# Kernel tuning notes

Measured on AMD Instinct MI355X. Metric: run time of the kernel, lower is better.

## Reference

```python
import jax, jax.numpy as jnp
import numpy as np
from jax import lax

B, C_IN, T = 1024, 9, 2048
RT = T // 4            # reduced timesteps after two MaxPool(2)
HID, OUT = 128, 64
N_NODES = B * RT


def _chain_edges(rt, batch):
    """Bidirectional chain graph per sample, offset per batch element (PyG fallback)."""
    i = np.arange(rt - 1)
    src = np.concatenate([i, i + 1])   # edge_index[0] = source j
    dst = np.concatenate([i + 1, i])   # edge_index[1] = target i
    off = (np.arange(batch) * rt)[:, None]
    src = (src[None, :] + off).reshape(-1)
    dst = (dst[None, :] + off).reshape(-1)
    # degree with self-loops (GCNConv adds self-loops): endpoints 2, interior 3
    deg = np.full(rt, 3.0, np.float32)
    deg[0] = deg[-1] = 2.0
    deg = np.tile(deg, batch)
    return jnp.asarray(src, jnp.int32), jnp.asarray(dst, jnp.int32), jnp.asarray(deg ** -0.5)


def _conv1d(x, w, b):
    # x: [B, Cin, T], w: [Cout, Cin, 5] -> [B, Cout, T] (padding=2)
    y = lax.conv_general_dilated(x, w, window_strides=(1,), padding=[(2, 2)],
                                 dimension_numbers=('NCH', 'OIH', 'NCH'))
    return y + b[None, :, None]


def _maxpool2(x):
    b, c, t = x.shape
    return x.reshape(b, c, t // 2, 2).max(axis=-1)


def _gcn(x, W, b, src, dst, dinv):
    # GCNConv: x' = D^-1/2 (A+I) D^-1/2 (x W) + b
    h = x @ W                                        # [N, F]
    norm_e = (dinv[src] * dinv[dst])[:, None]        # per-edge sym norm
    agg = jax.ops.segment_sum(h[src] * norm_e, dst, num_segments=h.shape[0])
    return agg + h * (dinv * dinv)[:, None] + b      # self-loop term: 1/deg


def setup_inputs() -> dict:
    key = jax.random.key(0)
    ks = jax.random.split(key, 12)
    s = lambda k, shp, sc: jax.random.normal(k, shp, jnp.float32) * sc
    return {
        'x': jax.random.normal(ks[0], (B, C_IN, T), jnp.float32),
        'conv1_w': s(ks[1], (16, C_IN, 5), 0.15), 'conv1_b': jnp.zeros((16,), jnp.float32),
        'conv2_w': s(ks[2], (32, 16, 5), 0.1),   'conv2_b': jnp.zeros((32,), jnp.float32),
        'gcn1_w': s(ks[3], (32, HID), 0.17),     'gcn1_b': jnp.zeros((HID,), jnp.float32),
        'gcn2_w': s(ks[4], (HID, HID), 0.09),    'gcn2_b': jnp.zeros((HID,), jnp.float32),
        'fc_w': s(ks[5], (HID, OUT), 0.09),      'fc_b': jnp.zeros((OUT,), jnp.float32),
    }


def reference(x, conv1_w, conv1_b, conv2_w, conv2_b,
              gcn1_w, gcn1_b, gcn2_w, gcn2_b, fc_w, fc_b):
    b, c, t = x.shape
    h = _maxpool2(jax.nn.relu(_conv1d(x, conv1_w, conv1_b)))   # [B,16,T/2]
    h = _maxpool2(jax.nn.relu(_conv1d(h, conv2_w, conv2_b)))   # [B,32,T/4]
    rt = h.shape[-1]
    h = jnp.transpose(h, (0, 2, 1)).reshape(b * rt, 32)        # [N,32]
    src, dst, dinv = _chain_edges(rt, b)
    h = jax.nn.relu(_gcn(h, gcn1_w, gcn1_b, src, dst, dinv))
    h = jax.nn.relu(_gcn(h, gcn2_w, gcn2_b, src, dst, dinv))
    h = h.reshape(b, rt, -1).mean(axis=1)                      # [B,HID]
    return h @ fc_w + fc_b                                     # [B,OUT]
```

## Files before the change

### kernel.cpp

```cpp
#include <hip/hip_runtime.h>
#include <hip/hip_bf16.h>

#define B_      1024
#define CIN     9
#define T0_     2048
#define C1_     16
#define C2_     32
#define RT_     512
#define NNODES  (B_ * RT_)
#define HID_    128
#define OUTF_   64

typedef __attribute__((ext_vector_type(8))) __bf16 bf16x8;
typedef __attribute__((ext_vector_type(4))) float f32x4;
typedef __attribute__((ext_vector_type(8))) unsigned short us8;

__device__ __forceinline__ float bf2f(unsigned short u) {
    union { unsigned int i; float f; } c; c.i = ((unsigned int)u) << 16; return c.f;
}
__device__ __forceinline__ unsigned short f2bf(float f) {
    union { float f; unsigned int i; } c; c.f = f;
    unsigned int i = c.i + 0x7FFFu + ((c.i >> 16) & 1u);
    return (unsigned short)(i >> 16);
}
__device__ __forceinline__ float dinv_of(int r) {
    return (r == 0 || r == RT_ - 1) ? 0.70710678118f : 0.57735026919f;
}

__global__ __launch_bounds__(256) void repack_w(
    const float* __restrict__ W1g, const float* __restrict__ W2g,
    const float* __restrict__ Wc1g, const float* __restrict__ Wc2g,
    unsigned short* __restrict__ Wb1, unsigned short* __restrict__ Wb2,
    unsigned short* __restrict__ Wc1, unsigned short* __restrict__ Wc2)
{
    const int tid = threadIdx.x;
    const int bid = blockIdx.x;
    if (bid == 0) {
        for (int s = tid; s < 32 * 128; s += 256) {
            int k = s >> 7, f = s & 127;
            int lane = ((k >> 3) << 4) + (f & 15);
            int e = (((f >> 4) * 64) + lane) * 8 + (k & 7);
            Wb1[e] = f2bf(W1g[s]);
        }
    } else if (bid <= 4) {
        const int s0 = (bid - 1) * 4096;
        for (int i = tid; i < 4096; i += 256) {
            int s = s0 + i;
            int k = s >> 7, f = s & 127;
            int ks = k >> 5, lane = (((k >> 3) & 3) << 4) + (f & 15);
            int e = ((ks * 8 + (f >> 4)) * 64 + lane) * 8 + (k & 7);
            Wb2[e] = f2bf(W2g[s]);
        }
    } else if (bid == 5) {
        for (int e = tid; e < 3 * 64 * 8; e += 256) {
            int j = e & 7, lane = (e >> 3) & 63, ks = e >> 9;
            int kk = ks * 32 + (lane >> 4) * 8 + j;
            int k = kk >> 4, ci = kk & 15, co = lane & 15;
            Wc1[e] = (k < 5 && ci < CIN) ? f2bf(Wc1g[(co * CIN + ci) * 5 + k]) : 0;
        }
    } else {
        for (int e = tid; e < 3 * 2 * 64 * 8; e += 256) {
            int j = e & 7, lane = (e >> 3) & 63, nt = (e >> 9) & 1, ks = e >> 10;
            int kk = ks * 32 + (lane >> 4) * 8 + j;
            int k = kk >> 4, ci = kk & 15, co = nt * 16 + (lane & 15);
            Wc2[e] = (k < 5) ? f2bf(Wc2g[(co * C1_ + ci) * 5 + k]) : 0;
        }
    }
}

__global__ __launch_bounds__(256, 2) void mega(
    const float* __restrict__ x,
    const unsigned short* __restrict__ Wc1,
    const unsigned short* __restrict__ Wc2,
    const unsigned short* __restrict__ Wb1,
    const unsigned short* __restrict__ Wb2,
    const float* __restrict__ c1b, const float* __restrict__ c2b,
    const float* __restrict__ g1b, const float* __restrict__ g2b,
    float* __restrict__ partials)
{
    __shared__ __align__(16) unsigned char lds[75808];
    unsigned short* xs    = (unsigned short*)(lds);
    unsigned short* As1   = (unsigned short*)(lds);
    unsigned short* y2loc = (unsigned short*)(lds + 11520);
    unsigned short* A2    = (unsigned short*)(lds);
    unsigned short* y1ext = (unsigned short*)(lds + 39424);
    unsigned short* H     = (unsigned short*)(lds + 39424);
    float* bls1 = (float*)(lds + 74784);
    float* bls2 = (float*)(lds + 75296);

    const int tid = threadIdx.x;
    const int b = blockIdx.x >> 2;
    const int r0 = (blockIdx.x & 3) * 128;
    const int n0 = blockIdx.x * 128;
    if (tid < 128) { bls1[tid] = g1b[tid]; bls2[tid] = g2b[tid]; }

    const int lane = tid & 63, wave = tid >> 6;
    const int m = lane & 15, q = lane >> 4;

    {
        const float* xb = x + (size_t)b * CIN * T0_;
        const int xbase = 4 * r0 - 14;
        for (int s = tid; s < 552; s += 256) {
            const int xt = xbase + s;
            us8 o0, o1;
            if (xt >= 0 && xt < T0_) {
                #pragma unroll
                for (int ci = 0; ci < 8; ci++) o0[ci] = f2bf(xb[ci * T0_ + xt]);
                o1[0] = f2bf(xb[8 * T0_ + xt]);
                #pragma unroll
                for (int jj = 1; jj < 8; jj++) o1[jj] = 0;
            } else {
                #pragma unroll
                for (int jj = 0; jj < 8; jj++) { o0[jj] = 0; o1[jj] = 0; }
            }
            *(us8*)(xs + s * 24) = o0;
            *(us8*)(xs + s * 24 + 8) = o1;
        }
    }
    __syncthreads();

    {
        bf16x8 wf[3];
        #pragma unroll
        for (int ks = 0; ks < 3; ks++) wf[ks] = *(const bf16x8*)(Wc1 + (ks * 64 + lane) * 8);
        const float bv = c1b[m];
        const int t1base = 2 * r0 - 6;
        for (int mt = wave; mt < 34; mt += 4) {
            f32x4 acc = {};
            #pragma unroll
            for (int ks = 0; ks < 3; ks++) {
                const int row = mt * 16 + m + ks * 2 + (q >> 1);
                const bf16x8 af = *(const bf16x8*)(xs + row * 24 + (q & 1) * 8);
                acc = __builtin_amdgcn_mfma_f32_16x16x32_bf16(af, wf[ks], acc, 0, 0, 0);
            }
            const int prow = mt * 8 + q * 2;
            const int t1a = t1base + prow, t1b = t1a + 1;
            const float p0 = fmaxf(fmaxf(acc[0], acc[1]) + bv, 0.f);
            const float p1 = fmaxf(fmaxf(acc[2], acc[3]) + bv, 0.f);
            if (prow < 268)
                y1ext[prow * 16 + m] = (t1a >= 0 && t1a < 1024) ? f2bf(p0) : (unsigned short)0;
            if (prow + 1 < 268)
                y1ext[(prow + 1) * 16 + m] = (t1b >= 0 && t1b < 1024) ? f2bf(p1) : (unsigned short)0;
        }
        for (int idx = tid; idx < 192; idx += 256) y1ext[268 * 16 + idx] = 0;
    }
    __syncthreads();

    {
        bf16x8 wf[3][2];
        #pragma unroll
        for (int ks = 0; ks < 3; ks++)
            #pragma unroll
            for (int nt = 0; nt < 2; nt++)
                wf[ks][nt] = *(const bf16x8*)(Wc2 + ((ks * 2 + nt) * 64 + lane) * 8);
        const float bv0 = c2b[m], bv1 = c2b[16 + m];
        for (int mt = wave; mt < 17; mt += 4) {
            f32x4 a0 = {}, a1 = {};
            #pragma unroll
            for (int ks = 0; ks < 3; ks++) {
                const int row = mt * 16 + m + ks * 2 + (q >> 1);
                const bf16x8 af = *(const bf16x8*)(y1ext + row * 16 + (q & 1) * 8);
                a0 = __builtin_amdgcn_mfma_f32_16x16x32_bf16(af, wf[ks][0], a0, 0, 0, 0);
                a1 = __builtin_amdgcn_mfma_f32_16x16x32_bf16(af, wf[ks][1], a1, 0, 0, 0);
            }
            const int nrow = mt * 8 + q * 2;
            if (nrow < 132) {
                y2loc[nrow * 32 + m]      = f2bf(fmaxf(fmaxf(a0[0], a0[1]) + bv0, 0.f));
                y2loc[nrow * 32 + 16 + m] = f2bf(fmaxf(fmaxf(a1[0], a1[1]) + bv1, 0.f));
            }
            if (nrow + 1 < 132) {
                y2loc[(nrow + 1) * 32 + m]      = f2bf(fmaxf(fmaxf(a0[2], a0[3]) + bv0, 0.f));
                y2loc[(nrow + 1) * 32 + 16 + m] = f2bf(fmaxf(fmaxf(a1[2], a1[3]) + bv1, 0.f));
            }
        }
    }
    __syncthreads();

    for (int s = tid; s < 288; s += 256) {
        const int i = s >> 1, fh = (s & 1) * 16;
        unsigned short* dst = As1 + i * 40 + fh;
        const int r = r0 - 1 + i;
        if (i >= 130 || r < 0 || r >= RT_) {
            us8 z;
            #pragma unroll
            for (int j = 0; j < 8; j++) z[j] = 0;
            *(us8*)dst = z; *(us8*)(dst + 8) = z;
        } else {
            const float dm = dinv_of(r), cm = dm * dm;
            const unsigned short* Yc = y2loc + (i + 1) * 32 + fh;
            us8 c0 = *(const us8*)(Yc), c1 = *(const us8*)(Yc + 8);
            float v[16];
            #pragma unroll
            for (int j = 0; j < 8; j++) { v[j] = cm * bf2f(c0[j]); v[8 + j] = cm * bf2f(c1[j]); }
            if (r > 0) {
                const float cl = dm * dinv_of(r - 1);
                us8 a0 = *(const us8*)(Yc - 32), a1 = *(const us8*)(Yc - 24);
                #pragma unroll
                for (int j = 0; j < 8; j++) { v[j] += cl * bf2f(a0[j]); v[8 + j] += cl * bf2f(a1[j]); }
            }
            if (r < RT_ - 1) {
                const float cr = dm * dinv_of(r + 1);
                us8 a0 = *(const us8*)(Yc + 32), a1 = *(const us8*)(Yc + 40);
                #pragma unroll
                for (int j = 0; j < 8; j++) { v[j] += cr * bf2f(a0[j]); v[8 + j] += cr * bf2f(a1[j]); }
            }
            us8 o0, o1;
            #pragma unroll
            for (int j = 0; j < 8; j++) { o0[j] = f2bf(v[j]); o1[j] = f2bf(v[8 + j]); }
            *(us8*)dst = o0; *(us8*)(dst + 8) = o1;
        }
    }
    __syncthreads();

    {
        const int ft0 = wave * 2;
        const bf16x8 wf0 = *(const bf16x8*)(Wb1 + (ft0 * 64 + lane) * 8);
        const bf16x8 wf1 = *(const bf16x8*)(Wb1 + ((ft0 + 1) * 64 + lane) * 8);
        const float4 bv0 = *(const float4*)&bls1[ft0 * 16 + q * 4];
        const float4 bv1 = *(const float4*)&bls1[(ft0 + 1) * 16 + q * 4];
        #pragma unroll
        for (int nt = 0; nt < 9; nt++) {
            const bf16x8 bfr = *(const bf16x8*)(As1 + (nt * 16 + m) * 40 + q * 8);
            f32x4 a0 = {}, a1 = {};
            a0 = __builtin_amdgcn_mfma_f32_16x16x32_bf16(wf0, bfr, a0, 0, 0, 0);
            a1 = __builtin_amdgcn_mfma_f32_16x16x32_bf16(wf1, bfr, a1, 0, 0, 0);
            const int row = nt * 16 + m;
            if (row < 130) {
                ushort4 o0, o1;
                o0.x = f2bf(fmaxf(a0[0] + bv0.x, 0.f));
                o0.y = f2bf(fmaxf(a0[1] + bv0.y, 0.f));
                o0.z = f2bf(fmaxf(a0[2] + bv0.z, 0.f));
                o0.w = f2bf(fmaxf(a0[3] + bv0.w, 0.f));
                o1.x = f2bf(fmaxf(a1[0] + bv1.x, 0.f));
                o1.y = f2bf(fmaxf(a1[1] + bv1.y, 0.f));
                o1.z = f2bf(fmaxf(a1[2] + bv1.z, 0.f));
                o1.w = f2bf(fmaxf(a1[3] + bv1.w, 0.f));
                *(ushort4*)(H + row * 136 + ft0 * 16 + q * 4) = o0;
                *(ushort4*)(H + row * 136 + (ft0 + 1) * 16 + q * 4) = o1;
            }
        }
    }
    __syncthreads();

    {
        const int j = tid >> 1, fh = (tid & 1) * 64;
        const int r = r0 + j;
        const float dm = dinv_of(r), cm = dm * dm;
        const float cl = (r > 0) ? dm * dinv_of(r - 1) : 0.f;
        const float cr = (r < RT_ - 1) ? dm * dinv_of(r + 1) : 0.f;
        const unsigned short* Hl = H + j * 136 + fh;
        const unsigned short* Hc = Hl + 136;
        const unsigned short* Hr = Hc + 136;
        unsigned short* dst = A2 + j * 152 + fh;
        #pragma unroll
        for (int c = 0; c < 8; c++) {
            us8 cc = *(const us8*)(Hc + c * 8);
            us8 ll = *(const us8*)(Hl + c * 8);
            us8 rr = *(const us8*)(Hr + c * 8);
            us8 o;
            #pragma unroll
            for (int e = 0; e < 8; e++)
                o[e] = f2bf(cm * bf2f(cc[e]) + cl * bf2f(ll[e]) + cr * bf2f(rr[e]));
            *(us8*)(dst + c * 8) = o;
        }
    }
    __syncthreads();

    bf16x8 bw[4][2];
    #pragma unroll
    for (int ks = 0; ks < 4; ks++)
        #pragma unroll
        for (int i = 0; i < 2; i++) {
            int ct = wave * 2 + i;
            bw[ks][i] = *(const bf16x8*)(Wb2 + ((size_t)((ks * 8 + ct) * 64 + lane)) * 8);
        }
    f32x4 acc[8][2] = {};
    #pragma unroll
    for (int ks = 0; ks < 4; ks++) {
        #pragma unroll
        for (int nt = 0; nt < 8; nt++) {
            const bf16x8 af = *(const bf16x8*)(A2 + (nt * 16 + m) * 152 + ks * 32 + q * 8);
            acc[nt][0] = __builtin_amdgcn_mfma_f32_16x16x32_bf16(af, bw[ks][0], acc[nt][0], 0, 0, 0);
            acc[nt][1] = __builtin_amdgcn_mfma_f32_16x16x32_bf16(af, bw[ks][1], acc[nt][1], 0, 0, 0);
        }
    }
    const float bb0 = bls2[wave * 32 + m];
    const float bb1 = bls2[wave * 32 + 16 + m];
    float s0 = 0.f, s1 = 0.f;
    #pragma unroll
    for (int nt = 0; nt < 8; nt++)
        #pragma unroll
        for (int rgi = 0; rgi < 4; rgi++) {
            s0 += fmaxf(acc[nt][0][rgi] + bb0, 0.f);
            s1 += fmaxf(acc[nt][1][rgi] + bb1, 0.f);
        }
    s0 += __shfl_xor(s0, 16, 64); s0 += __shfl_xor(s0, 32, 64);
    s1 += __shfl_xor(s1, 16, 64); s1 += __shfl_xor(s1, 32, 64);
    if (lane < 16) {
        float* p = partials + (size_t)blockIdx.x * 128 + wave * 32;
        p[m] = s0;
        p[16 + m] = s1;
    }
}

__global__ __launch_bounds__(128) void fc_kernel(
    const float* __restrict__ partials, const float* __restrict__ fw,
    const float* __restrict__ fb, float* __restrict__ out)
{
    __shared__ float sm[128];
    const int b = blockIdx.x, tid = threadIdx.x;
    float s = 0.f;
    #pragma unroll
    for (int t = 0; t < 4; t++) s += partials[((b << 2) + t) * 128 + tid];
    sm[tid] = s * (1.0f / 512.0f);
    __syncthreads();
    if (tid < 64) {
        float acc = fb[tid];
        #pragma unroll 8
        for (int f = 0; f < 128; f++) acc += sm[f] * fw[f * 64 + tid];
        out[b * 64 + tid] = acc;
    }
}

extern "C" void kernel_launch(void* const* d_in, const int* in_sizes, int n_in,
                              void* d_out, int out_size, void* d_ws, size_t ws_size,
                              hipStream_t stream)
{
    const float* x   = (const float*)d_in[0];
    const float* w1  = (const float*)d_in[1];
    const float* b1  = (const float*)d_in[2];
    const float* w2  = (const float*)d_in[3];
    const float* b2  = (const float*)d_in[4];
    const float* g1w = (const float*)d_in[5];
    const float* g1b = (const float*)d_in[6];
    const float* g2w = (const float*)d_in[7];
    const float* g2b = (const float*)d_in[8];
    const float* fw  = (const float*)d_in[9];
    const float* fb  = (const float*)d_in[10];

    char* ws = (char*)d_ws;
    const size_t MB = 1024 * 1024;
    float* partials     = (float*)(ws);
    unsigned short* Wb1 = (unsigned short*)(ws + 2 * MB);
    unsigned short* Wb2 = (unsigned short*)(ws + 2 * MB + 16 * 1024);
    unsigned short* Wc1 = (unsigned short*)(ws + 2 * MB + 64 * 1024);
    unsigned short* Wc2 = (unsigned short*)(ws + 2 * MB + 80 * 1024);
    float* out = (float*)d_out;

    repack_w<<<7, 256, 0, stream>>>(g1w, g2w, w1, w2, Wb1, Wb2, Wc1, Wc2);
    mega<<<NNODES / 128, 256, 0, stream>>>(x, Wc1, Wc2, Wb1, Wb2,
                                           b1, b2, g1b, g2b, partials);
    fc_kernel<<<B_, 128, 0, stream>>>(partials, fw, fb, out);
}
```

Measured before the change: 215.2 us.

## Fuse weight repack and FC head into mega kernel with last-block atomics

Drops the separate weight-repack and FC kernels. Each block now loads and packs its bf16 MFMA weight fragments straight from fp32 global memory, and the four blocks of a sample combine their means through atomics. The last block to arrive, found with a per-sample counter, runs the FC layer. Rounding switches to a cheaper round-half-up bf16 conversion done two values at a time with perm. This removes two launches and the partials round trip, but adds a memset, redundant per-block weight gathers and atomic contention.

Result: slower. 539.2 us (+150.6%).

```diff
diff --git a/kernel.cpp b/kernel.cpp
--- a/kernel.cpp
+++ b/kernel.cpp
@@ -18,65 +18,34 @@
 __device__ __forceinline__ float bf2f(unsigned short u) {
     union { unsigned int i; float f; } c; c.i = ((unsigned int)u) << 16; return c.f;
 }
-__device__ __forceinline__ unsigned short f2bf(float f) {
+__device__ __forceinline__ unsigned short f2bf1(float f) {
     union { float f; unsigned int i; } c; c.f = f;
-    unsigned int i = c.i + 0x7FFFu + ((c.i >> 16) & 1u);
-    return (unsigned short)(i >> 16);
+    return (unsigned short)((c.i + 0x8000u) >> 16);
+}
+__device__ __forceinline__ unsigned int f2bf2(float lo, float hi) {
+    union { float f; unsigned int i; } a, b; a.f = lo; b.f = hi;
+    return __builtin_amdgcn_perm(b.i + 0x8000u, a.i + 0x8000u, 0x07060302u);
+}
+__device__ __forceinline__ bf16x8 pack8(const float* v) {
+    union { bf16x8 h; unsigned int u[4]; } r;
+    #pragma unroll
+    for (int i = 0; i < 4; i++) r.u[i] = f2bf2(v[2 * i], v[2 * i + 1]);
+    return r.h;
 }
 __device__ __forceinline__ float dinv_of(int r) {
     return (r == 0 || r == RT_ - 1) ? 0.70710678118f : 0.57735026919f;
 }
 
-__global__ __launch_bounds__(256) void repack_w(
-    const float* __restrict__ W1g, const float* __restrict__ W2g,
-    const float* __restrict__ Wc1g, const float* __restrict__ Wc2g,
-    unsigned short* __restrict__ Wb1, unsigned short* __restrict__ Wb2,
-    unsigned short* __restrict__ Wc1, unsigned short* __restrict__ Wc2)
-{
-    const int tid = threadIdx.x;
-    const int bid = blockIdx.x;
-    if (bid == 0) {
-        for (int s = tid; s < 32 * 128; s += 256) {
-            int k = s >> 7, f = s & 127;
-            int lane = ((k >> 3) << 4) + (f & 15);
-            int e = (((f >> 4) * 64) + lane) * 8 + (k & 7);
-            Wb1[e] = f2bf(W1g[s]);
-        }
-    } else if (bid <= 4) {
-        const int s0 = (bid - 1) * 4096;
-        for (int i = tid; i < 4096; i += 256) {
-            int s = s0 + i;
-            int k = s >> 7, f = s & 127;
-            int ks = k >> 5, lane = (((k >> 3) & 3) << 4) + (f & 15);
-            int e = ((ks * 8 + (f >> 4)) * 64 + lane) * 8 + (k & 7);
-            Wb2[e] = f2bf(W2g[s]);
-        }
-    } else if (bid == 5) {
-        for (int e = tid; e < 3 * 64 * 8; e += 256) {
-            int j = e & 7, lane = (e >> 3) & 63, ks = e >> 9;
-            int kk = ks * 32 + (lane >> 4) * 8 + j;
-            int k = kk >> 4, ci = kk & 15, co = lane & 15;
-            Wc1[e] = (k < 5 && ci < CIN) ? f2bf(Wc1g[(co * CIN + ci) * 5 + k]) : 0;
-        }
-    } else {
-        for (int e = tid; e < 3 * 2 * 64 * 8; e += 256) {
-            int j = e & 7, lane = (e >> 3) & 63, nt = (e >> 9) & 1, ks = e >> 10;
-            int kk = ks * 32 + (lane >> 4) * 8 + j;
-            int k = kk >> 4, ci = kk & 15, co = nt * 16 + (lane & 15);
-            Wc2[e] = (k < 5) ? f2bf(Wc2g[(co * C1_ + ci) * 5 + k]) : 0;
-        }
-    }
-}
-
 __global__ __launch_bounds__(256, 2) void mega(
     const float* __restrict__ x,
-    const unsigned short* __restrict__ Wc1,
-    const unsigned short* __restrict__ Wc2,
-    const unsigned short* __restrict__ Wb1,
-    const unsigned short* __restrict__ Wb2,
-    const float* __restrict__ c1b, const float* __restrict__ c2b,
-    const float* __restrict__ g1b, const float* __restrict__ g2b,
-    float* __restrict__ partials)
+    const float* __restrict__ w1c, const float* __restrict__ c1b,
+    const float* __restrict__ w2c, const float* __restrict__ c2b,
+    const float* __restrict__ g1w, const float* __restrict__ g1b,
+    const float* __restrict__ g2w, const float* __restrict__ g2b,
+    const float* __restrict__ fcw, const float* __restrict__ fcb,
+    float* __restrict__ accum,
+    unsigned int* __restrict__ cnt,
+    float* __restrict__ outp)
 {
     __shared__ __align__(16) unsigned char lds[75808];
     unsigned short* xs    = (unsigned short*)(lds);
@@ -91,38 +60,60 @@
     const int tid = threadIdx.x;
     const int b = blockIdx.x >> 2;
     const int r0 = (blockIdx.x & 3) * 128;
-    const int n0 = blockIdx.x * 128;
     if (tid < 128) { bls1[tid] = g1b[tid]; bls2[tid] = g2b[tid]; }
 
     const int lane = tid & 63, wave = tid >> 6;
     const int m = lane & 15, q = lane >> 4;
+
+    bf16x8 wfB[3];
+    #pragma unroll
+    for (int ks = 0; ks < 3; ks++) {
+        float v[8];
+        #pragma unroll
+        for (int j = 0; j < 8; j++) {
+            int kk = ks * 32 + q * 8 + j, kt = kk >> 4, ci = kk & 15;
+            v[j] = (kt < 5 && ci < CIN) ? w1c[(m * CIN + ci) * 5 + kt] : 0.f;
+        }
+        wfB[ks] = pack8(v);
+    }
+    bf16x8 wfC[3][2];
+    #pragma unroll
+    for (int ks = 0; ks < 3; ks++)
+        #pragma unroll
+        for (int nt = 0; nt < 2; nt++) {
+            float v[8];
+            #pragma unroll
+            for (int j = 0; j < 8; j++) {
+                int kk = ks * 32 + q * 8 + j, kt = kk >> 4, ci = kk & 15;
+                v[j] = (kt < 5) ? w2c[((nt * 16 + m) * C1_ + ci) * 5 + kt] : 0.f;
+            }
+            wfC[ks][nt] = pack8(v);
+        }
 
     {
         const float* xb = x + (size_t)b * CIN * T0_;
         const int xbase = 4 * r0 - 14;
         for (int s = tid; s < 552; s += 256) {
             const int xt = xbase + s;
-            us8 o0, o1;
+            union { us8 v; unsigned int u[4]; } o0, o1;
             if (xt >= 0 && xt < T0_) {
+                float xv[9];
                 #pragma unroll
-                for (int ci = 0; ci < 8; ci++) o0[ci] = f2bf(xb[ci * T0_ + xt]);
-                o1[0] = f2bf(xb[8 * T0_ + xt]);
-                #pragma unroll
-                for (int jj = 1; jj < 8; jj++) o1[jj] = 0;
+                for (int ci = 0; ci < 9; ci++) xv[ci] = xb[ci * T0_ + xt];
+                o0.u[0] = f2bf2(xv[0], xv[1]); o0.u[1] = f2bf2(xv[2], xv[3]);
+                o0.u[2] = f2bf2(xv[4], xv[5]); o0.u[3] = f2bf2(xv[6], xv[7]);
+                o1.u[0] = f2bf2(xv[8], 0.f);   o1.u[1] = o1.u[2] = o1.u[3] = 0;
             } else {
-                #pragma unroll
-                for (int jj = 0; jj < 8; jj++) { o0[jj] = 0; o1[jj] = 0; }
-            }
-            *(us8*)(xs + s * 24) = o0;
-            *(us8*)(xs + s * 24 + 8) = o1;
-        }
-    }
-    __syncthreads();
-
-    {
-        bf16x8 wf[3];
-        #pragma unroll
-        for (int ks = 0; ks < 3; ks++) wf[ks] = *(const bf16x8*)(Wc1 + (ks * 64 + lane) * 8);
+                o0.u[0] = o0.u[1] = o0.u[2] = o0.u[3] = 0;
+                o1.u[0] = o1.u[1] = o1.u[2] = o1.u[3] = 0;
+            }
+            *(us8*)(xs + s * 24) = o0.v;
+            *(us8*)(xs + s * 24 + 8) = o1.v;
+        }
+    }
+    __syncthreads();
+
+    {
         const float bv = c1b[m];
         const int t1base = 2 * r0 - 6;
         for (int mt = wave; mt < 34; mt += 4) {
@@ -131,28 +122,22 @@
             for (int ks = 0; ks < 3; ks++) {
                 const int row = mt * 16 + m + ks * 2 + (q >> 1);
                 const bf16x8 af = *(const bf16x8*)(xs + row * 24 + (q & 1) * 8);
-                acc = __builtin_amdgcn_mfma_f32_16x16x32_bf16(af, wf[ks], acc, 0, 0, 0);
+                acc = __builtin_amdgcn_mfma_f32_16x16x32_bf16(af, wfB[ks], acc, 0, 0, 0);
             }
             const int prow = mt * 8 + q * 2;
             const int t1a = t1base + prow, t1b = t1a + 1;
             const float p0 = fmaxf(fmaxf(acc[0], acc[1]) + bv, 0.f);
             const float p1 = fmaxf(fmaxf(acc[2], acc[3]) + bv, 0.f);
             if (prow < 268)
-                y1ext[prow * 16 + m] = (t1a >= 0 && t1a < 1024) ? f2bf(p0) : (unsigned short)0;
+                y1ext[prow * 16 + m] = (t1a >= 0 && t1a < 1024) ? f2bf1(p0) : (unsigned short)0;
             if (prow + 1 < 268)
-                y1ext[(prow + 1) * 16 + m] = (t1b >= 0 && t1b < 1024) ? f2bf(p1) : (unsigned short)0;
+                y1ext[(prow + 1) * 16 + m] = (t1b >= 0 && t1b < 1024) ? f2bf1(p1) : (unsigned short)0;
         }
         for (int idx = tid; idx < 192; idx += 256) y1ext[268 * 16 + idx] = 0;
     }
     __syncthreads();
 
     {
-        bf16x8 wf[3][2];
-        #pragma unroll
-        for (int ks = 0; ks < 3; ks++)
-            #pragma unroll
-            for (int nt = 0; nt < 2; nt++)
-                wf[ks][nt] = *(const bf16x8*)(Wc2 + ((ks * 2 + nt) * 64 + lane) * 8);
         const float bv0 = c2b[m], bv1 = c2b[16 + m];
         for (int mt = wave; mt < 17; mt += 4) {
             f32x4 a0 = {}, a1 = {};
@@ -160,18 +145,30 @@
             for (int ks = 0; ks < 3; ks++) {
                 const int row = mt * 16 + m + ks * 2 + (q >> 1);
                 const bf16x8 af = *(const bf16x8*)(y1ext + row * 16 + (q & 1) * 8);
-                a0 = __builtin_amdgcn_mfma_f32_16x16x32_bf16(af, wf[ks][0], a0, 0, 0, 0);
-                a1 = __builtin_amdgcn_mfma_f32_16x16x32_bf16(af, wf[ks][1], a1, 0, 0, 0);
+                a0 = __builtin_amdgcn_mfma_f32_16x16x32_bf16(af, wfC[ks][0], a0, 0, 0, 0);
+                a1 = __builtin_amdgcn_mfma_f32_16x16x32_bf16(af, wfC[ks][1], a1, 0, 0, 0);
             }
             const int nrow = mt * 8 + q * 2;
             if (nrow < 132) {
-                y2loc[nrow * 32 + m]      = f2bf(fmaxf(fmaxf(a0[0], a0[1]) + bv0, 0.f));
-                y2loc[nrow * 32 + 16 + m] = f2bf(fmaxf(fmaxf(a1[0], a1[1]) + bv1, 0.f));
+                y2loc[nrow * 32 + m]      = f2bf1(fmaxf(fmaxf(a0[0], a0[1]) + bv0, 0.f));
+                y2loc[nrow * 32 + 16 + m] = f2bf1(fmaxf(fmaxf(a1[0], a1[1]) + bv1, 0.f));
             }
             if (nrow + 1 < 132) {
-                y2loc[(nrow + 1) * 32 + m]      = f2bf(fmaxf(fmaxf(a0[2], a0[3]) + bv0, 0.f));
-                y2loc[(nrow + 1) * 32 + 16 + m] = f2bf(fmaxf(fmaxf(a1[2], a1[3]) + bv1, 0.f));
-            }
+                y2loc[(nrow + 1) * 32 + m]      = f2bf1(fmaxf(fmaxf(a0[2], a0[3]) + bv0, 0.f));
+                y2loc[(nrow + 1) * 32 + 16 + m] = f2bf1(fmaxf(fmaxf(a1[2], a1[3]) + bv1, 0.f));
+            }
+        }
+    }
+    bf16x8 wfE[2];
+    {
+        const int ft0 = wave * 2;
+        #pragma unroll
+        for (int i = 0; i < 2; i++) {
+            float v[8];
+            #pragma unroll
+            for (int j = 0; j < 8; j++)
+                v[j] = g1w[(q * 8 + j) * 128 + (ft0 + i) * 16 + m];
+            wfE[i] = pack8(v);
         }
     }
     __syncthreads();
@@ -180,11 +177,10 @@
         const int i = s >> 1, fh = (s & 1) * 16;
         unsigned short* dst = As1 + i * 40 + fh;
         const int r = r0 - 1 + i;
+        union { us8 v; unsigned int u[4]; } o0, o1;
         if (i >= 130 || r < 0 || r >= RT_) {
-            us8 z;
-            #pragma unroll
-            for (int j = 0; j < 8; j++) z[j] = 0;
-            *(us8*)dst = z; *(us8*)(dst + 8) = z;
+            o0.u[0] = o0.u[1] = o0.u[2] = o0.u[3] = 0;
+            o1.u[0] = o1.u[1] = o1.u[2] = o1.u[3] = 0;
         } else {
             const float dm = dinv_of(r), cm = dm * dm;
             const unsigned short* Yc = y2loc + (i + 1) * 32 + fh;
@@ -204,39 +200,46 @@
                 #pragma unroll
                 for (int j = 0; j < 8; j++) { v[j] += cr * bf2f(a0[j]); v[8 + j] += cr * bf2f(a1[j]); }
             }
-            us8 o0, o1;
-            #pragma unroll
-            for (int j = 0; j < 8; j++) { o0[j] = f2bf(v[j]); o1[j] = f2bf(v[8 + j]); }
-            *(us8*)dst = o0; *(us8*)(dst + 8) = o1;
-        }
-    }
+            #pragma unroll
+            for (int i2 = 0; i2 < 4; i2++) {
+                o0.u[i2] = f2bf2(v[2 * i2], v[2 * i2 + 1]);
+                o1.u[i2] = f2bf2(v[8 + 2 * i2], v[9 + 2 * i2]);
+            }
+        }
+        *(us8*)dst = o0.v; *(us8*)(dst + 8) = o1.v;
+    }
+    bf16x8 bw[4][2];
+    #pragma unroll
+    for (int ks = 0; ks < 4; ks++)
+        #pragma unroll
+        for (int i = 0; i < 2; i++) {
+            float v[8];
+            #pragma unroll
+            for (int j = 0; j < 8; j++)
+                v[j] = g2w[(ks * 32 + q * 8 + j) * 128 + (wave * 2 + i) * 16 + m];
+            bw[ks][i] = pack8(v);
+        }
     __syncthreads();
 
     {
         const int ft0 = wave * 2;
-        const bf16x8 wf0 = *(const bf16x8*)(Wb1 + (ft0 * 64 + lane) * 8);
-        const bf16x8 wf1 = *(const bf16x8*)(Wb1 + ((ft0 + 1) * 64 + lane) * 8);
         const float4 bv0 = *(const float4*)&bls1[ft0 * 16 + q * 4];
         const float4 bv1 = *(const float4*)&bls1[(ft0 + 1) * 16 + q * 4];
         #pragma unroll
         for (int nt = 0; nt < 9; nt++) {
             const bf16x8 bfr = *(const bf16x8*)(As1 + (nt * 16 + m) * 40 + q * 8);
             f32x4 a0 = {}, a1 = {};
-            a0 = __builtin_amdgcn_mfma_f32_16x16x32_bf16(wf0, bfr, a0, 0, 0, 0);
-            a1 = __builtin_amdgcn_mfma_f32_16x16x32_bf16(wf1, bfr, a1, 0, 0, 0);
+            a0 = __builtin_amdgcn_mfma_f32_16x16x32_bf16(wfE[0], bfr, a0, 0, 0, 0);
+            a1 = __builtin_amdgcn_mfma_f32_16x16x32_bf16(wfE[1], bfr, a1, 0, 0, 0);
             const int row = nt * 16 + m;
             if (row < 130) {
-                ushort4 o0, o1;
-                o0.x = f2bf(fmaxf(a0[0] + bv0.x, 0.f));
-                o0.y = f2bf(fmaxf(a0[1] + bv0.y, 0.f));
-                o0.z = f2bf(fmaxf(a0[2] + bv0.z, 0.f));
-                o0.w = f2bf(fmaxf(a0[3] + bv0.w, 0.f));
-                o1.x = f2bf(fmaxf(a1[0] + bv1.x, 0.f));
-                o1.y = f2bf(fmaxf(a1[1] + bv1.y, 0.f));
-                o1.z = f2bf(fmaxf(a1[2] + bv1.z, 0.f));
-                o1.w = f2bf(fmaxf(a1[3] + bv1.w, 0.f));
-                *(ushort4*)(H + row * 136 + ft0 * 16 + q * 4) = o0;
-                *(ushort4*)(H + row * 136 + (ft0 + 1) * 16 + q * 4) = o1;
+                union { ushort4 s; unsigned int u[2]; } o0, o1;
+                o0.u[0] = f2bf2(fmaxf(a0[0] + bv0.x, 0.f), fmaxf(a0[1] + bv0.y, 0.f));
+                o0.u[1] = f2bf2(fmaxf(a0[2] + bv0.z, 0.f), fmaxf(a0[3] + bv0.w, 0.f));
+                o1.u[0] = f2bf2(fmaxf(a1[0] + bv1.x, 0.f), fmaxf(a1[1] + bv1.y, 0.f));
+                o1.u[1] = f2bf2(fmaxf(a1[2] + bv1.z, 0.f), fmaxf(a1[3] + bv1.w, 0.f));
+                *(ushort4*)(H + row * 136 + ft0 * 16 + q * 4) = o0.s;
+                *(ushort4*)(H + row * 136 + (ft0 + 1) * 16 + q * 4) = o1.s;
             }
         }
     }
@@ -257,23 +260,18 @@
             us8 cc = *(const us8*)(Hc + c * 8);
             us8 ll = *(const us8*)(Hl + c * 8);
             us8 rr = *(const us8*)(Hr + c * 8);
-            us8 o;
+            float v[8];
             #pragma unroll
             for (int e = 0; e < 8; e++)
-                o[e] = f2bf(cm * bf2f(cc[e]) + cl * bf2f(ll[e]) + cr * bf2f(rr[e]));
-            *(us8*)(dst + c * 8) = o;
-        }
-    }
-    __syncthreads();
-
-    bf16x8 bw[4][2];
-    #pragma unroll
-    for (int ks = 0; ks < 4; ks++)
-        #pragma unroll
-        for (int i = 0; i < 2; i++) {
-            int ct = wave * 2 + i;
-            bw[ks][i] = *(const bf16x8*)(Wb2 + ((size_t)((ks * 8 + ct) * 64 + lane)) * 8);
-        }
+                v[e] = cm * bf2f(cc[e]) + cl * bf2f(ll[e]) + cr * bf2f(rr[e]);
+            union { us8 v; unsigned int u[4]; } o;
+            #pragma unroll
+            for (int i2 = 0; i2 < 4; i2++) o.u[i2] = f2bf2(v[2 * i2], v[2 * i2 + 1]);
+            *(us8*)(dst + c * 8) = o.v;
+        }
+    }
+    __syncthreads();
+
     f32x4 acc[8][2] = {};
     #pragma unroll
     for (int ks = 0; ks < 4; ks++) {
@@ -284,41 +282,44 @@
             acc[nt][1] = __builtin_amdgcn_mfma_f32_16x16x32_bf16(af, bw[ks][1], acc[nt][1], 0, 0, 0);
         }
     }
-    const float bb0 = bls2[wave * 32 + m];
-    const float bb1 = bls2[wave * 32 + 16 + m];
-    float s0 = 0.f, s1 = 0.f;
-    #pragma unroll
-    for (int nt = 0; nt < 8; nt++)
-        #pragma unroll
-        for (int rgi = 0; rgi < 4; rgi++) {
-            s0 += fmaxf(acc[nt][0][rgi] + bb0, 0.f);
-            s1 += fmaxf(acc[nt][1][rgi] + bb1, 0.f);
-        }
-    s0 += __shfl_xor(s0, 16, 64); s0 += __shfl_xor(s0, 32, 64);
-    s1 += __shfl_xor(s1, 16, 64); s1 += __shfl_xor(s1, 32, 64);
-    if (lane < 16) {
-        float* p = partials + (size_t)blockIdx.x * 128 + wave * 32;
-        p[m] = s0;
-        p[16 + m] = s1;
-    }
-}
-
-__global__ __launch_bounds__(128) void fc_kernel(
-    const float* __restrict__ partials, const float* __restrict__ fw,
-    const float* __restrict__ fb, float* __restrict__ out)
-{
-    __shared__ float sm[128];
-    const int b = blockIdx.x, tid = threadIdx.x;
-    float s = 0.f;
-    #pragma unroll
-    for (int t = 0; t < 4; t++) s += partials[((b << 2) + t) * 128 + tid];
-    sm[tid] = s * (1.0f / 512.0f);
-    __syncthreads();
-    if (tid < 64) {
-        float acc = fb[tid];
-        #pragma unroll 8
-        for (int f = 0; f < 128; f++) acc += sm[f] * fw[f * 64 + tid];
-        out[b * 64 + tid] = acc;
+    {
+        const float bb0 = bls2[wave * 32 + m];
+        const float bb1 = bls2[wave * 32 + 16 + m];
+        float s0 = 0.f, s1 = 0.f;
+        #pragma unroll
+        for (int nt = 0; nt < 8; nt++)
+            #pragma unroll
+            for (int rgi = 0; rgi < 4; rgi++) {
+                s0 += fmaxf(acc[nt][0][rgi] + bb0, 0.f);
+                s1 += fmaxf(acc[nt][1][rgi] + bb1, 0.f);
+            }
+        s0 += __shfl_xor(s0, 16, 64); s0 += __shfl_xor(s0, 32, 64);
+        s1 += __shfl_xor(s1, 16, 64); s1 += __shfl_xor(s1, 32, 64);
+        if (lane < 16) {
+            atomicAdd(accum + b * 128 + wave * 32 + m, s0);
+            atomicAdd(accum + b * 128 + wave * 32 + 16 + m, s1);
+        }
+    }
+
+    __threadfence();
+    __syncthreads();
+    volatile int* flag = (volatile int*)(lds + 512);
+    if (tid == 0) {
+        unsigned int old = atomicAdd(cnt + b, 1u);
+        *flag = (old == 3u) ? 1 : 0;
+    }
+    __syncthreads();
+    if (*flag) {
+        float* smf = (float*)lds;
+        if (tid < 128)
+            smf[tid] = atomicAdd(accum + b * 128 + tid, 0.0f) * (1.0f / 512.0f);
+        __syncthreads();
+        if (tid < 64) {
+            float a = fcb[tid];
+            #pragma unroll 8
+            for (int f = 0; f < 128; f++) a += smf[f] * fcw[f * 64 + tid];
+            outp[b * 64 + tid] = a;
+        }
     }
 }
 
@@ -339,16 +340,12 @@
     const float* fb  = (const float*)d_in[10];
 
     char* ws = (char*)d_ws;
-    const size_t MB = 1024 * 1024;
-    float* partials     = (float*)(ws);
-    unsigned short* Wb1 = (unsigned short*)(ws + 2 * MB);
-    unsigned short* Wb2 = (unsigned short*)(ws + 2 * MB + 16 * 1024);
-    unsigned short* Wc1 = (unsigned short*)(ws + 2 * MB + 64 * 1024);
-    unsigned short* Wc2 = (unsigned short*)(ws + 2 * MB + 80 * 1024);
+    float* accum       = (float*)(ws);
+    unsigned int* cnt  = (unsigned int*)(ws + 524288);
     float* out = (float*)d_out;
 
-    repack_w<<<7, 256, 0, stream>>>(g1w, g2w, w1, w2, Wb1, Wb2, Wc1, Wc2);
-    mega<<<NNODES / 128, 256, 0, stream>>>(x, Wc1, Wc2, Wb1, Wb2,
-                                           b1, b2, g1b, g2b, partials);
-    fc_kernel<<<B_, 128, 0, stream>>>(partials, fw, fb, out);
-}
+    hipMemsetAsync(d_ws, 0, 524288 + 4096, stream);
+    mega<<<NNODES / 128, 256, 0, stream>>>(x, w1, b1, w2, b2,
+                                           g1w, g1b, g2w, g2b, fw, fb,
+                                           accum, cnt, out);
+}
```
